# Kernel optimization log

Hardware: AMD Instinct MI355X
Metric: run time of the kernel (lower is better)

The kernel has to match this reference:

```python
import jax, jax.numpy as jnp
import numpy as np

B, N, M, C, H = 8, 1024, 128, 1024, 16
D = C // H
MLP = int(C * 4.0)
EPS = 1e-6


def setup_inputs() -> dict:
    key = jax.random.key(0)
    ks = jax.random.split(key, 24)
    def w(k, shape):
        return jax.random.normal(k, shape, jnp.float32) * 0.02
    mask = jax.random.randint(ks[3], (B, M), 0, 2, dtype=jnp.int32)
    mask = mask.at[:, 0].set(1)  # ensure at least one attendable token per row
    return {
        "x": jax.random.normal(ks[0], (B, N, C), jnp.float32),
        "c_dino": jax.random.normal(ks[1], (B, C), jnp.float32),
        "c_text": jax.random.normal(ks[2], (B, M, C), jnp.float32),
        "text_mask": mask,
        "W_ada": w(ks[4], (C, 6 * C)), "b_ada": jnp.zeros((6 * C,), jnp.float32),
        "W_qkv": w(ks[5], (C, 3 * C)), "b_qkv": jnp.zeros((3 * C,), jnp.float32),
        "W_proj_sa": w(ks[6], (C, C)), "b_proj_sa": jnp.zeros((C,), jnp.float32),
        "W_q": w(ks[7], (C, C)), "b_q": jnp.zeros((C,), jnp.float32),
        "W_kv": w(ks[8], (C, 2 * C)), "b_kv": jnp.zeros((2 * C,), jnp.float32),
        "W_proj_ca": w(ks[9], (C, C)), "b_proj_ca": jnp.zeros((C,), jnp.float32),
        "W_fc1": w(ks[10], (C, MLP)), "b_fc1": jnp.zeros((MLP,), jnp.float32),
        "W_fc2": w(ks[11], (MLP, C)), "b_fc2": jnp.zeros((C,), jnp.float32),
    }


def _ln(x):
    # LayerNorm without affine params, eps=1e-6
    mu = jnp.mean(x, axis=-1, keepdims=True)
    xc = x - mu
    var = jnp.mean(xc * xc, axis=-1, keepdims=True)
    return xc * jax.lax.rsqrt(var + EPS)


def _modulate(x, shift, scale):
    return x * (1.0 + scale[:, None, :]) + shift[:, None, :]


def _heads(t):
    b, n, _ = t.shape
    return t.reshape(b, n, H, D)


def reference(x, c_dino, c_text, text_mask,
              W_ada, b_ada, W_qkv, b_qkv, W_proj_sa, b_proj_sa,
              W_q, b_q, W_kv, b_kv, W_proj_ca, b_proj_ca,
              W_fc1, b_fc1, W_fc2, b_fc2):
    scale = D ** (-0.5)
    ada = jax.nn.silu(c_dino) @ W_ada + b_ada  # (B, 6C)
    sh_msa, sc_msa, sh_ca, sc_ca, sh_mlp, sc_mlp = jnp.split(ada, 6, axis=1)

    # --- self-attention ---
    h = _modulate(_ln(x), sh_msa, sc_msa)
    qkv = h @ W_qkv + b_qkv
    q, k, v = (_heads(t) for t in jnp.split(qkv, 3, axis=-1))  # (B,N,H,D)
    attn = jax.nn.softmax(jnp.einsum('bnhd,bmhd->bhnm', q, k) * scale, axis=-1)
    sa = jnp.einsum('bhnm,bmhd->bnhd', attn, v).reshape(B, N, C) @ W_proj_sa + b_proj_sa
    x = x + sa

    # --- cross-attention ---
    h = _modulate(_ln(x), sh_ca, sc_ca)
    q = _heads(h @ W_q + b_q)                 # (B,N,H,D)
    kv = c_text @ W_kv + b_kv
    k, v = (_heads(t) for t in jnp.split(kv, 2, axis=-1))  # (B,M,H,D)
    scores = jnp.einsum('bnhd,bmhd->bhnm', q, k) * scale
    scores = jnp.where(text_mask[:, None, None, :] == 0, -jnp.inf, scores)
    attn = jax.nn.softmax(scores, axis=-1)
    ca = jnp.einsum('bhnm,bmhd->bnhd', attn, v).reshape(B, N, C) @ W_proj_ca + b_proj_ca
    x = x + ca

    # --- MLP ---
    h = _modulate(_ln(x), sh_mlp, sc_mlp)
    mlp = jax.nn.gelu(h @ W_fc1 + b_fc1, approximate=True) @ W_fc2 + b_fc2
    return x + mlp
```

## Files before the change

### kernel.cpp

```cpp
#include <hip/hip_runtime.h>
#include <hip/hip_bf16.h>

#define B_   8
#define N_   1024
#define M_   128
#define C_   1024
#define H_   16
#define D_   64
#define MLP_ 4096

typedef __bf16 bf16;
typedef __bf16 bf16x8 __attribute__((ext_vector_type(8)));
typedef __bf16 bf16x4 __attribute__((ext_vector_type(4)));
typedef float  f32x4  __attribute__((ext_vector_type(4)));

__device__ __forceinline__ f32x4 mfma16(bf16x8 a, bf16x8 b, f32x4 c) {
    return __builtin_amdgcn_mfma_f32_16x16x32_bf16(a, b, c, 0, 0, 0);
}

__device__ __forceinline__ void gload16(const bf16* g, bf16* l) {
    __builtin_amdgcn_global_load_lds(
        (const __attribute__((address_space(1))) void*)g,
        (__attribute__((address_space(3))) void*)l, 16, 0, 0);
}

__global__ __launch_bounds__(256) void transpose_k(const float* __restrict__ W,
                                                   bf16* __restrict__ Wt,
                                                   int K, int Nc) {
    __shared__ float tile[32][33];
    const int x  = threadIdx.x & 31;
    const int y0 = threadIdx.x >> 5;
    const size_t n0 = (size_t)blockIdx.x * 32;
    const size_t k0 = (size_t)blockIdx.y * 32;
#pragma unroll
    for (int i = 0; i < 4; i++)
        tile[y0 + i * 8][x] = W[(k0 + y0 + i * 8) * Nc + n0 + x];
    __syncthreads();
#pragma unroll
    for (int i = 0; i < 4; i++)
        Wt[(n0 + y0 + i * 8) * K + k0 + x] = (bf16)tile[x][y0 + i * 8];
}

__global__ __launch_bounds__(256) void vtrans_k(const bf16* __restrict__ in, int instride,
                                                int coff, int Mk, bf16* __restrict__ outT) {
    __shared__ bf16 t[32][33];
    const int tx = threadIdx.x & 31;
    const int ty0 = threadIdx.x >> 5;
    const int m0  = blockIdx.x * 32;
    const int hd0 = blockIdx.y * 32;
    const int b   = blockIdx.z;
#pragma unroll
    for (int i = 0; i < 4; i++)
        t[ty0 + i * 8][tx] = in[((size_t)(b * Mk + m0 + ty0 + i * 8)) * instride + coff + hd0 + tx];
    __syncthreads();
#pragma unroll
    for (int i = 0; i < 4; i++)
        outT[((size_t)(b * 1024 + hd0 + ty0 + i * 8)) * Mk + m0 + tx] = t[tx][ty0 + i * 8];
}

__global__ __launch_bounds__(256) void cvt_bf16_k(const float* __restrict__ in,
                                                  bf16* __restrict__ out, int n4) {
    int i = blockIdx.x * 256 + threadIdx.x;
    if (i < n4) {
        float4 v = ((const float4*)in)[i];
        bf16x4 o;
        o[0] = (bf16)v.x; o[1] = (bf16)v.y; o[2] = (bf16)v.z; o[3] = (bf16)v.w;
        ((bf16x4*)out)[i] = o;
    }
}

__global__ __launch_bounds__(256) void ada_init_k(const float* __restrict__ bias,
                                                  float* __restrict__ ada) {
    int i = blockIdx.x * 256 + threadIdx.x;
    ada[i] = bias[i % 6144];
}

__global__ __launch_bounds__(256) void ada_k(const float* __restrict__ cdino,
                                             const float* __restrict__ W,
                                             float* __restrict__ ada) {
    __shared__ float sc[8][32];
    const int tid = threadIdx.x;
    const int k0  = blockIdx.y * 32;
    {
        float c = cdino[(tid >> 5) * 1024 + k0 + (tid & 31)];
        sc[tid >> 5][tid & 31] = c / (1.f + __expf(-c));
    }
    __syncthreads();
    const int col = blockIdx.x * 256 + tid;
    float acc[8];
#pragma unroll
    for (int b = 0; b < 8; b++) acc[b] = 0.f;
    for (int kk = 0; kk < 32; kk++) {
        float w = W[(size_t)(k0 + kk) * 6144 + col];
#pragma unroll
        for (int b = 0; b < 8; b++) acc[b] += sc[b][kk] * w;
    }
#pragma unroll
    for (int b = 0; b < 8; b++) atomicAdd(&ada[(size_t)b * 6144 + col], acc[b]);
}

__global__ __launch_bounds__(256) void ln_mod_k(const float* __restrict__ X,
                                                const float* __restrict__ ada,
                                                int shoff, int scoff,
                                                bf16* __restrict__ Hout) {
    const int row = blockIdx.x;
    const int b   = row >> 10;
    const int tid = threadIdx.x;
    const float4 v = ((const float4*)(X + (size_t)row * C_))[tid];
    float s  = v.x + v.y + v.z + v.w;
    float sq = v.x * v.x + v.y * v.y + v.z * v.z + v.w * v.w;
#pragma unroll
    for (int off = 32; off; off >>= 1) {
        s  += __shfl_xor(s,  off);
        sq += __shfl_xor(sq, off);
    }
    __shared__ float rs_[4], rq_[4];
    if ((tid & 63) == 0) { rs_[tid >> 6] = s; rq_[tid >> 6] = sq; }
    __syncthreads();
    s  = rs_[0] + rs_[1] + rs_[2] + rs_[3];
    sq = rq_[0] + rq_[1] + rq_[2] + rq_[3];
    const float mu   = s * (1.f / 1024.f);
    const float var  = sq * (1.f / 1024.f) - mu * mu;
    const float rstd = rsqrtf(var + 1e-6f);
    const float4 scv = ((const float4*)(ada + (size_t)b * 6144 + scoff))[tid];
    const float4 shv = ((const float4*)(ada + (size_t)b * 6144 + shoff))[tid];
    bf16x4 o;
    o[0] = (bf16)(((v.x - mu) * rstd) * (1.f + scv.x) + shv.x);
    o[1] = (bf16)(((v.y - mu) * rstd) * (1.f + scv.y) + shv.y);
    o[2] = (bf16)(((v.z - mu) * rstd) * (1.f + scv.z) + shv.z);
    o[3] = (bf16)(((v.w - mu) * rstd) * (1.f + scv.w) + shv.w);
    *(bf16x4*)(Hout + (size_t)row * C_ + tid * 4) = o;
}

template <int MODE, int KS>
__global__ __launch_bounds__(256 * KS) void gemm_k(const bf16* __restrict__ A,
                                                   const bf16* __restrict__ Bt,
                                                   const float* __restrict__ bias,
                                                   const float* resid,
                                                   float* outF, bf16* outB,
                                                   int Ncols, int K, int GX) {
    __shared__ __attribute__((aligned(16))) bf16 As[2][KS][128][32];
    __shared__ __attribute__((aligned(16))) bf16 Bs[2][KS][128][32];
    const int tid  = threadIdx.x & 255;
    const int grp  = threadIdx.x >> 8;
    const int lane = tid & 63, wave = tid >> 6;
    const int lrow = lane & 15, quad = lane >> 4;
    const int wm = wave >> 1, wn = wave & 1;

    const unsigned lid = blockIdx.x;
    const unsigned xcd = lid & 7, s = lid >> 3;
    const unsigned bnb = s % GX, bmb = (s / GX) * 8 + xcd;
    const size_t bm = (size_t)bmb * 128;
    const size_t bn = (size_t)bnb * 128;

    const int Kh = K / KS;
    const int prow = tid >> 2, pseg = tid & 3;
    const int gseg = pseg ^ ((prow >> 1) & 3);
    const bf16* gA0 = A  + (bm + prow) * (size_t)K + grp * Kh + gseg * 8;
    const bf16* gA1 = gA0 + (size_t)64 * K;
    const bf16* gB0 = Bt + (bn + prow) * (size_t)K + grp * Kh + gseg * 8;
    const bf16* gB1 = gB0 + (size_t)64 * K;
    const int bufoff = KS * 128 * 32;
    bf16* lA = &As[0][grp][0][0] + wave * 512;
    bf16* lB = &Bs[0][grp][0][0] + wave * 512;

    const int xoff = (quad ^ ((lrow >> 1) & 3)) * 8;

    f32x4 acc[4][4];
#pragma unroll
    for (int i = 0; i < 4; i++)
#pragma unroll
        for (int j = 0; j < 4; j++) acc[i][j] = (f32x4){0.f, 0.f, 0.f, 0.f};

    {
        gload16(gA0, lA);
        gload16(gA1, lA + 2048);
        gload16(gB0, lB);
        gload16(gB1, lB + 2048);
    }
    int p = 0;
    for (int ko = 0; ko < Kh; ko += 32) {
        __syncthreads();
        if (ko + 32 < Kh) {
            const int po = (p ^ 1) * bufoff;
            gload16(gA0 + ko + 32, lA + po);
            gload16(gA1 + ko + 32, lA + po + 2048);
            gload16(gB0 + ko + 32, lB + po);
            gload16(gB1 + ko + 32, lB + po + 2048);
        }
        const bf16(*Asp)[32] = As[p][grp];
        const bf16(*Bsp)[32] = Bs[p][grp];
        bf16x8 af[4], bfr[4];
#pragma unroll
        for (int mi = 0; mi < 4; mi++)
            af[mi] = *(const bf16x8*)&Asp[wm * 64 + mi * 16 + lrow][xoff];
#pragma unroll
        for (int ni = 0; ni < 4; ni++)
            bfr[ni] = *(const bf16x8*)&Bsp[wn * 64 + ni * 16 + lrow][xoff];
#pragma unroll
        for (int mi = 0; mi < 4; mi++)
#pragma unroll
            for (int ni = 0; ni < 4; ni++)
                acc[mi][ni] = mfma16(af[mi], bfr[ni], acc[mi][ni]);
        p ^= 1;
    }

    if constexpr (KS == 2) {
        f32x4* red = (f32x4*)&As[0][0][0][0];
#pragma unroll
        for (int rnd = 0; rnd < 4; rnd++) {
            __syncthreads();
            if (grp == 1) {
#pragma unroll
                for (int c = 0; c < 4; c++) {
                    const int idx = rnd * 4 + c;
                    red[c * 256 + tid] = acc[idx >> 2][idx & 3];
                }
            }
            __syncthreads();
            if (grp == 0) {
#pragma unroll
                for (int c = 0; c < 4; c++) {
                    const int idx = rnd * 4 + c;
                    acc[idx >> 2][idx & 3] += red[c * 256 + tid];
                }
            }
        }
    }

    if (grp == 0) {
#pragma unroll
        for (int mi = 0; mi < 4; mi++) {
#pragma unroll
            for (int ni = 0; ni < 4; ni++) {
                const size_t gcol = bn + wn * 64 + ni * 16 + lrow;
                const float bv = bias[gcol];
#pragma unroll
                for (int r = 0; r < 4; r++) {
                    const size_t grow = bm + wm * 64 + mi * 16 + quad * 4 + r;
                    const size_t idx  = grow * Ncols + gcol;
                    float v = acc[mi][ni][r] + bv;
                    if (MODE == 1) {
                        outF[idx] = v + resid[idx];
                    } else if (MODE == 2) {
                        outB[idx] = (bf16)v;
                    } else {
                        float z = 1.59576912f * (v + 0.044715f * v * v * v);
                        outB[idx] = (bf16)(v / (1.f + __expf(-z)));
                    }
                }
            }
        }
    }
}

template <bool MASKED>
__global__ __launch_bounds__(256) void attn_k(const bf16* __restrict__ Qp, int qstride,
                                              const bf16* __restrict__ Kp, int kstride,
                                              const bf16* __restrict__ Vtg,
                                              const int* __restrict__ mask, int Mk,
                                              bf16* __restrict__ O) {
    __shared__ __attribute__((aligned(16))) bf16 Kt[64][88];
    __shared__ __attribute__((aligned(16))) bf16 Vt[64][88];
    __shared__ __attribute__((aligned(16))) bf16 Pt[4][16][88];
    __shared__ float madd[64];

    const int b = blockIdx.z, h = blockIdx.y;
    const int tid  = threadIdx.x;
    const int lane = tid & 63, wave = tid >> 6;
    const int lrow = lane & 15, quad = lane >> 4;
    const int q0 = blockIdx.x * 64 + wave * 16;

    const bf16* qp = Qp + ((size_t)(b * N_ + q0 + lrow)) * qstride + h * 64 + quad * 8;
    const bf16x8 bq0 = *(const bf16x8*)(qp);
    const bf16x8 bq1 = *(const bf16x8*)(qp + 32);

    f32x4 acc[4];
#pragma unroll
    for (int t = 0; t < 4; t++) acc[t] = (f32x4){0.f, 0.f, 0.f, 0.f};
    float mrun = -3e38f, lrun = 0.f;

    const int srow = tid >> 2;
    const int sseg = (tid & 3) * 16;

    const bf16* kbase = Kp + ((size_t)b * Mk + srow) * kstride + h * 64 + sseg;
    const bf16* vbase = Vtg + ((size_t)(b * 1024 + h * 64 + srow)) * Mk + sseg;

    for (int kc = 0; kc < Mk; kc += 64) {
        __syncthreads();
        const bf16* kp = kbase + (size_t)kc * kstride;
        bf16x8 k0 = *(const bf16x8*)kp;
        bf16x8 k1 = *(const bf16x8*)(kp + 8);
        *(bf16x8*)&Kt[srow][sseg]     = k0;
        *(bf16x8*)&Kt[srow][sseg + 8] = k1;
        const bf16* vp = vbase + kc;
        bf16x8 v0 = *(const bf16x8*)vp;
        bf16x8 v1 = *(const bf16x8*)(vp + 8);
        *(bf16x8*)&Vt[srow][sseg]     = v0;
        *(bf16x8*)&Vt[srow][sseg + 8] = v1;
        if (MASKED && tid < 64)
            madd[tid] = (mask[b * Mk + kc + tid] == 0) ? -1e30f : 0.f;
        __syncthreads();

        float sv[4][4];
#pragma unroll
        for (int t = 0; t < 4; t++) {
            f32x4 s = (f32x4){0.f, 0.f, 0.f, 0.f};
            bf16x8 ak0 = *(const bf16x8*)&Kt[t * 16 + lrow][quad * 8];
            s = mfma16(ak0, bq0, s);
            bf16x8 ak1 = *(const bf16x8*)&Kt[t * 16 + lrow][32 + quad * 8];
            s = mfma16(ak1, bq1, s);
#pragma unroll
            for (int r = 0; r < 4; r++) {
                float ma = MASKED ? madd[t * 16 + quad * 4 + r] : 0.f;
                sv[t][r] = s[r] * 0.125f + ma;
            }
        }

        float vmax = sv[0][0];
#pragma unroll
        for (int t = 0; t < 4; t++)
#pragma unroll
            for (int r = 0; r < 4; r++) vmax = fmaxf(vmax, sv[t][r]);
        vmax = fmaxf(vmax, __shfl_xor(vmax, 16));
        vmax = fmaxf(vmax, __shfl_xor(vmax, 32));
        const float mnew  = fmaxf(mrun, vmax);
        const float alpha = __expf(mrun - mnew);
        mrun = mnew;
        float rsum = 0.f;
#pragma unroll
        for (int t = 0; t < 4; t++) {
            bf16x4 p4;
#pragma unroll
            for (int r = 0; r < 4; r++) {
                float p = __expf(sv[t][r] - mnew);
                rsum += p;
                p4[r] = (bf16)p;
            }
            *(bf16x4*)&Pt[wave][lrow][t * 16 + quad * 4] = p4;
        }
        rsum += __shfl_xor(rsum, 16);
        rsum += __shfl_xor(rsum, 32);
        lrun = lrun * alpha + rsum;

        float alpha4[4];
#pragma unroll
        for (int r = 0; r < 4; r++) alpha4[r] = __shfl(alpha, quad * 4 + r);
#pragma unroll
        for (int t = 0; t < 4; t++)
#pragma unroll
            for (int r = 0; r < 4; r++) acc[t][r] *= alpha4[r];

        __syncthreads();
        const bf16x8 ap0 = *(const bf16x8*)&Pt[wave][lrow][quad * 8];
        const bf16x8 ap1 = *(const bf16x8*)&Pt[wave][lrow][32 + quad * 8];

#pragma unroll
        for (int t = 0; t < 4; t++) {
            bf16x8 bv0 = *(const bf16x8*)&Vt[t * 16 + lrow][quad * 8];
            acc[t] = mfma16(ap0, bv0, acc[t]);
            bf16x8 bv1 = *(const bf16x8*)&Vt[t * 16 + lrow][32 + quad * 8];
            acc[t] = mfma16(ap1, bv1, acc[t]);
        }
    }

    float linv = 1.f / lrun;
    float linv4[4];
#pragma unroll
    for (int r = 0; r < 4; r++) linv4[r] = __shfl(linv, quad * 4 + r);
#pragma unroll
    for (int r = 0; r < 4; r++) {
        const size_t grow = (size_t)(b * N_ + q0 + quad * 4 + r);
#pragma unroll
        for (int t = 0; t < 4; t++)
            O[grow * C_ + h * 64 + t * 16 + lrow] = (bf16)(acc[t][r] * linv4[r]);
    }
}

extern "C" void kernel_launch(void* const* d_in, const int* in_sizes, int n_in,
                              void* d_out, int out_size, void* d_ws, size_t ws_size,
                              hipStream_t stream) {
    const float* x     = (const float*)d_in[0];
    const float* cdino = (const float*)d_in[1];
    const float* ctext = (const float*)d_in[2];
    const int*   tmask = (const int*)d_in[3];
    const float* W_ada = (const float*)d_in[4];
    const float* b_ada = (const float*)d_in[5];
    const float* W_qkv = (const float*)d_in[6];
    const float* b_qkv = (const float*)d_in[7];
    const float* W_sa  = (const float*)d_in[8];
    const float* b_sa  = (const float*)d_in[9];
    const float* W_q   = (const float*)d_in[10];
    const float* b_q   = (const float*)d_in[11];
    const float* W_kv  = (const float*)d_in[12];
    const float* b_kv  = (const float*)d_in[13];
    const float* W_ca  = (const float*)d_in[14];
    const float* b_ca  = (const float*)d_in[15];
    const float* W_fc1 = (const float*)d_in[16];
    const float* b_fc1 = (const float*)d_in[17];
    const float* W_fc2 = (const float*)d_in[18];
    const float* b_fc2 = (const float*)d_in[19];
    float* out = (float*)d_out;

    char* ws = (char*)d_ws;
    size_t off = 0;
    auto alloc = [&](size_t bytes) -> char* {
        char* p = ws + off;
        off += (bytes + 255) & ~(size_t)255;
        return p;
    };
    float* ada  = (float*)alloc((size_t)8 * 6144 * 4);
    bf16* ctxb  = (bf16*)alloc((size_t)1024 * 1024 * 2);
    bf16* WqkvT = (bf16*)alloc((size_t)3072 * 1024 * 2);
    bf16* WsaT  = (bf16*)alloc((size_t)1024 * 1024 * 2);
    bf16* WqT   = (bf16*)alloc((size_t)1024 * 1024 * 2);
    bf16* WkvT  = (bf16*)alloc((size_t)2048 * 1024 * 2);
    bf16* WcaT  = (bf16*)alloc((size_t)1024 * 1024 * 2);
    bf16* Wfc1T = (bf16*)alloc((size_t)4096 * 1024 * 2);
    bf16* Wfc2T = (bf16*)alloc((size_t)1024 * 4096 * 2);
    float* xbuf = (float*)alloc((size_t)8192 * 1024 * 4);
    bf16* hbuf  = (bf16*)alloc((size_t)8192 * 1024 * 2);
    bf16* attnb = (bf16*)alloc((size_t)8192 * 1024 * 2);
    bf16* VtgSA = (bf16*)alloc((size_t)8192 * 1024 * 2);
    bf16* VtgCA = (bf16*)alloc((size_t)8192 * 128 * 2);
    bf16* pool  = (bf16*)alloc((size_t)8192 * 4096 * 2);
    if (off > ws_size) return;

    bf16* qkvb  = pool;
    bf16* qb    = pool;
    bf16* kvb   = pool + (size_t)8192 * 1024;
    bf16* gelub = pool;

    transpose_k<<<dim3(3072 / 32, 1024 / 32), 256, 0, stream>>>(W_qkv, WqkvT, 1024, 3072);
    transpose_k<<<dim3(1024 / 32, 1024 / 32), 256, 0, stream>>>(W_sa,  WsaT,  1024, 1024);
    transpose_k<<<dim3(1024 / 32, 1024 / 32), 256, 0, stream>>>(W_q,   WqT,   1024, 1024);
    transpose_k<<<dim3(2048 / 32, 1024 / 32), 256, 0, stream>>>(W_kv,  WkvT,  1024, 2048);
    transpose_k<<<dim3(1024 / 32, 1024 / 32), 256, 0, stream>>>(W_ca,  WcaT,  1024, 1024);
    transpose_k<<<dim3(4096 / 32, 1024 / 32), 256, 0, stream>>>(W_fc1, Wfc1T, 1024, 4096);
    transpose_k<<<dim3(1024 / 32, 4096 / 32), 256, 0, stream>>>(W_fc2, Wfc2T, 4096, 1024);
    cvt_bf16_k<<<1024, 256, 0, stream>>>(ctext, ctxb, 262144);

    ada_init_k<<<192, 256, 0, stream>>>(b_ada, ada);
    ada_k<<<dim3(24, 32), 256, 0, stream>>>(cdino, W_ada, ada);

    ln_mod_k<<<8192, 256, 0, stream>>>(x, ada, 0, 1024, hbuf);
    gemm_k<2, 1><<<24 * 64, 256, 0, stream>>>(hbuf, WqkvT, b_qkv, nullptr, nullptr, qkvb, 3072, 1024, 24);
    vtrans_k<<<dim3(32, 32, 8), 256, 0, stream>>>(qkvb, 3072, 2048, 1024, VtgSA);
    attn_k<false><<<dim3(16, 16, 8), 256, 0, stream>>>(qkvb, 3072, qkvb + 1024, 3072, VtgSA,
                                                       nullptr, 1024, attnb);
    gemm_k<1, 2><<<8 * 64, 512, 0, stream>>>(attnb, WsaT, b_sa, x, xbuf, nullptr, 1024, 1024, 8);

    ln_mod_k<<<8192, 256, 0, stream>>>(xbuf, ada, 2048, 3072, hbuf);
    gemm_k<2, 2><<<8 * 64, 512, 0, stream>>>(hbuf, WqT, b_q, nullptr, nullptr, qb, 1024, 1024, 8);
    gemm_k<2, 2><<<16 * 8, 512, 0, stream>>>(ctxb, WkvT, b_kv, nullptr, nullptr, kvb, 2048, 1024, 16);
    vtrans_k<<<dim3(4, 32, 8), 256, 0, stream>>>(kvb, 2048, 1024, 128, VtgCA);
    attn_k<true><<<dim3(16, 16, 8), 256, 0, stream>>>(qb, 1024, kvb, 2048, VtgCA,
                                                      tmask, 128, attnb);
    gemm_k<1, 2><<<8 * 64, 512, 0, stream>>>(attnb, WcaT, b_ca, xbuf, xbuf, nullptr, 1024, 1024, 8);

    ln_mod_k<<<8192, 256, 0, stream>>>(xbuf, ada, 4096, 5120, hbuf);
    gemm_k<3, 1><<<32 * 64, 256, 0, stream>>>(hbuf, Wfc1T, b_fc1, nullptr, nullptr, gelub, 4096, 1024, 32);
    gemm_k<1, 2><<<8 * 64, 512, 0, stream>>>(gelub, Wfc2T, b_fc2, xbuf, out, nullptr, 1024, 4096, 8);
}
```

Baseline: 713.3 us.

## Add 256x256-tile GEMM kernel for QKV and FC1 projections

Adds a new bf16 MFMA GEMM kernel with 256x256 output tiles, 8 waves each computing a 128x64 sub-tile, double-buffered LDS staging via global_load_lds with XOR swizzle, and s_setprio around the MFMA burst. The QKV and FC1 GEMMs (the largest N dimensions) now use it instead of the 128x128 kernel. The aim is higher arithmetic intensity and fewer global/LDS loads per FLOP. In exchange it uses many more accumulator registers and fewer blocks (384 and 512), which may hurt occupancy or wave balance across CUs.

```diff
diff --git a/kernel.cpp b/kernel.cpp
--- a/kernel.cpp
+++ b/kernel.cpp
@@ -130,6 +130,116 @@
     o[2] = (bf16)(((v.z - mu) * rstd) * (1.f + scv.z) + shv.z);
     o[3] = (bf16)(((v.w - mu) * rstd) * (1.f + scv.w) + shv.w);
     *(bf16x4*)(Hout + (size_t)row * C_ + tid * 4) = o;
+}
+
+template <int MODE>
+__global__ __launch_bounds__(512, 2) void gemm256_k(const bf16* __restrict__ A,
+                                                    const bf16* __restrict__ Bt,
+                                                    const float* __restrict__ bias,
+                                                    bf16* __restrict__ outB,
+                                                    int Ncols, int K, int GX) {
+    __shared__ __attribute__((aligned(16))) bf16 As[2][2][256][32];
+    __shared__ __attribute__((aligned(16))) bf16 Bs[2][2][256][32];
+
+    const int tid  = threadIdx.x;
+    const int lane = tid & 63, wave = tid >> 6;
+    const int lrow = lane & 15, quad = lane >> 4;
+    const int wm = wave >> 2, wn = wave & 3;
+
+    const unsigned lid = blockIdx.x;
+    const unsigned cpx = gridDim.x >> 3;
+    const unsigned g   = (lid & 7) * cpx + (lid >> 3);
+    const size_t bm = (size_t)(g / GX) * 256;
+    const size_t bn = (size_t)(g % GX) * 256;
+
+    const int r0 = tid >> 2;
+    const int cs = ((tid & 3) ^ (r0 & 3)) * 8;
+    const bf16* gA0 = A  + (bm + r0) * (size_t)K + cs;
+    const bf16* gA1 = gA0 + (size_t)128 * K;
+    const bf16* gB0 = Bt + (bn + r0) * (size_t)K + cs;
+    const bf16* gB1 = gB0 + (size_t)128 * K;
+
+    f32x4 acc[8][4];
+#pragma unroll
+    for (int i = 0; i < 8; i++)
+#pragma unroll
+        for (int j = 0; j < 4; j++) acc[i][j] = (f32x4){0.f, 0.f, 0.f, 0.f};
+
+    auto stage = [&](int bb, int ks, int koff) {
+        bf16* la = &As[bb][ks][0][0] + wave * 512;
+        bf16* lb = &Bs[bb][ks][0][0] + wave * 512;
+        gload16(gA0 + koff, la);
+        gload16(gA1 + koff, la + 4096);
+        gload16(gB0 + koff, lb);
+        gload16(gB1 + koff, lb + 4096);
+    };
+
+    const int xo = (quad ^ (lrow & 3)) * 8;
+
+    auto compute = [&](int bb, int ks) {
+        const bf16(*Ap)[32] = As[bb][ks];
+        const bf16(*Bp)[32] = Bs[bb][ks];
+        bf16x8 bq[4], af[8];
+#pragma unroll
+        for (int ni = 0; ni < 4; ni++)
+            bq[ni] = *(const bf16x8*)&Bp[wn * 64 + ni * 16 + lrow][xo];
+#pragma unroll
+        for (int mi = 0; mi < 8; mi++)
+            af[mi] = *(const bf16x8*)&Ap[wm * 128 + mi * 16 + lrow][xo];
+        __builtin_amdgcn_s_barrier();
+        __builtin_amdgcn_s_setprio(1);
+#pragma unroll
+        for (int mi = 0; mi < 8; mi++)
+#pragma unroll
+            for (int ni = 0; ni < 4; ni++)
+                acc[mi][ni] = mfma16(af[mi], bq[ni], acc[mi][ni]);
+        __builtin_amdgcn_s_setprio(0);
+    };
+
+    stage(0, 0, 0);
+    stage(0, 1, 32);
+    asm volatile("s_waitcnt vmcnt(4)" ::: "memory");
+    __builtin_amdgcn_s_barrier();
+
+    const int KT = K >> 6;
+    for (int kt = 0; kt < KT - 1; ++kt) {
+        const int b  = kt & 1;
+        const int kn = (kt + 1) << 6;
+        stage(b ^ 1, 0, kn);
+        compute(b, 0);
+        asm volatile("s_waitcnt vmcnt(4)" ::: "memory");
+        __builtin_amdgcn_s_barrier();
+        stage(b ^ 1, 1, kn + 32);
+        compute(b, 1);
+        asm volatile("s_waitcnt vmcnt(4)" ::: "memory");
+        __builtin_amdgcn_s_barrier();
+    }
+    {
+        const int b = (KT - 1) & 1;
+        compute(b, 0);
+        asm volatile("s_waitcnt vmcnt(0)" ::: "memory");
+        __builtin_amdgcn_s_barrier();
+        compute(b, 1);
+    }
+
+#pragma unroll
+    for (int mi = 0; mi < 8; mi++) {
+#pragma unroll
+        for (int ni = 0; ni < 4; ni++) {
+            const size_t gcol = bn + wn * 64 + ni * 16 + lrow;
+            const float bv = bias[gcol];
+#pragma unroll
+            for (int r = 0; r < 4; r++) {
+                const size_t grow = bm + wm * 128 + mi * 16 + quad * 4 + r;
+                float v = acc[mi][ni][r] + bv;
+                if (MODE == 3) {
+                    float z = 1.59576912f * (v + 0.044715f * v * v * v);
+                    v = v / (1.f + __expf(-z));
+                }
+                outB[grow * Ncols + gcol] = (bf16)v;
+            }
+        }
+    }
 }
 
 template <int MODE, int KS>
@@ -444,7 +554,7 @@
     ada_k<<<dim3(24, 32), 256, 0, stream>>>(cdino, W_ada, ada);
 
     ln_mod_k<<<8192, 256, 0, stream>>>(x, ada, 0, 1024, hbuf);
-    gemm_k<2, 1><<<24 * 64, 256, 0, stream>>>(hbuf, WqkvT, b_qkv, nullptr, nullptr, qkvb, 3072, 1024, 24);
+    gemm256_k<2><<<32 * 12, 512, 0, stream>>>(hbuf, WqkvT, b_qkv, qkvb, 3072, 1024, 12);
     vtrans_k<<<dim3(32, 32, 8), 256, 0, stream>>>(qkvb, 3072, 2048, 1024, VtgSA);
     attn_k<false><<<dim3(16, 16, 8), 256, 0, stream>>>(qkvb, 3072, qkvb + 1024, 3072, VtgSA,
                                                        nullptr, 1024, attnb);
@@ -459,6 +569,6 @@
     gemm_k<1, 2><<<8 * 64, 512, 0, stream>>>(attnb, WcaT, b_ca, xbuf, xbuf, nullptr, 1024, 1024, 8);
 
     ln_mod_k<<<8192, 256, 0, stream>>>(xbuf, ada, 4096, 5120, hbuf);
-    gemm_k<3, 1><<<32 * 64, 256, 0, stream>>>(hbuf, Wfc1T, b_fc1, nullptr, nullptr, gelub, 4096, 1024, 32);
+    gemm256_k<3><<<32 * 16, 512, 0, stream>>>(hbuf, Wfc1T, b_fc1, gelub, 4096, 1024, 16);
     gemm_k<1, 2><<<8 * 64, 512, 0, stream>>>(gelub, Wfc2T, b_fc2, xbuf, out, nullptr, 1024, 4096, 8);
 }
```

New measurement: 742.9 us. +4.2%, slower.
